# Kernel tuning notes

Hardware: AMD Instinct MI355X
Metric: run time of the kernel (lower is better)

Reference implementation:

```python
import jax, jax.numpy as jnp
import numpy as np

N_NODES = 50000
N_EDGES = 800000
D_IN = 128
D_HID = 128
N_CLASSES = 10


def setup_inputs() -> dict:
    key = jax.random.key(0)
    ks = jax.random.split(key, 8)
    x = jax.random.normal(ks[0], (N_NODES, D_IN), dtype=jnp.float32)
    edge_index = jax.random.randint(ks[1], (2, N_EDGES), 0, N_NODES, dtype=jnp.int64)
    s = 1.0 / np.sqrt(D_IN)
    W1 = jax.random.uniform(ks[2], (D_IN, D_HID), jnp.float32, -s, s)
    b1 = jnp.zeros((D_HID,), jnp.float32)
    W2 = jax.random.uniform(ks[3], (D_HID, D_HID), jnp.float32, -s, s)
    b2 = jnp.zeros((D_HID,), jnp.float32)
    sl = 1.0 / np.sqrt(D_HID)
    Wl = jax.random.uniform(ks[4], (D_HID, N_CLASSES), jnp.float32, -sl, sl)
    bl = jax.random.uniform(ks[5], (N_CLASSES,), jnp.float32, -sl, sl)
    return {"x": x, "edge_index": edge_index, "W1": W1, "b1": b1,
            "W2": W2, "b2": b2, "Wl": Wl, "bl": bl}


def gcn_conv(x, src, dst, W, b, n_nodes):
    # PyG GCNConv: add self-loops, symmetric normalization, gather-scatter aggregate
    h = x @ W                                             # [N, D_out]
    loop = jnp.arange(n_nodes, dtype=src.dtype)
    src2 = jnp.concatenate([src, loop])                   # [E+N]
    dst2 = jnp.concatenate([dst, loop])
    deg = jax.ops.segment_sum(jnp.ones_like(dst2, dtype=h.dtype), dst2,
                              num_segments=n_nodes)       # in-degree incl. self-loop
    dinv = jnp.where(deg > 0, jax.lax.rsqrt(deg), 0.0)
    norm = dinv[src2] * dinv[dst2]                        # [E+N]
    msgs = h[src2] * norm[:, None]                        # gather + scale  [E+N, D_out]
    out = jax.ops.segment_sum(msgs, dst2, num_segments=n_nodes)  # scatter-add
    return out + b


def reference(x, edge_index, W1, b1, W2, b2, Wl, bl):
    src, dst = edge_index[0], edge_index[1]
    n = x.shape[0]
    h = jax.nn.relu(gcn_conv(x, src, dst, W1, b1, n))     # dropout is identity in eval
    h = jax.nn.relu(gcn_conv(h, src, dst, W2, b2, n))
    logits = h @ Wl + bl                                  # [N, C]
    return jax.nn.log_softmax(logits, axis=1)
```

## Files before the change

### kernel.cpp

```cpp
#include <hip/hip_runtime.h>
#include <hip/hip_bf16.h>

#define D 128
#define NCLS 10

static __device__ __forceinline__ float relu(float x){ return fmaxf(x, 0.0f); }
static __device__ __forceinline__ float bf_lo(unsigned v){ return __uint_as_float(v << 16); }
static __device__ __forceinline__ float bf_hi(unsigned v){ return __uint_as_float(v & 0xffff0000u); }

__global__ __launch_bounds__(256) void k_zero_i32(int* __restrict__ p, int n){
  int i = blockIdx.x*256 + threadIdx.x;
  if (i < n) p[i] = 0;
}

__global__ __launch_bounds__(256) void k_hist(const int* __restrict__ dst,
                                              int* __restrict__ counts, int E){
  int i = blockIdx.x*256 + threadIdx.x;
  if (i < E) atomicAdd(counts + dst[i], 1);
}

__global__ __launch_bounds__(256) void k_scan1(const int* __restrict__ counts,
                                               int* __restrict__ rowPtr,
                                               int* __restrict__ bsum, int n){
  const int i = blockIdx.x*256 + threadIdx.x;
  const int lane = threadIdx.x & 63;
  const int wid  = threadIdx.x >> 6;
  int v = (i < n) ? counts[i] : 0;
  int s = v;
  #pragma unroll
  for (int off = 1; off < 64; off <<= 1){
    int u = __shfl_up(s, off, 64);
    if (lane >= off) s += u;
  }
  __shared__ int ws[4];
  if (lane == 63) ws[wid] = s;
  __syncthreads();
  int add = 0;
  if (wid >= 1) add += ws[0];
  if (wid >= 2) add += ws[1];
  if (wid >= 3) add += ws[2];
  int incl = s + add;
  if (i < n) rowPtr[i] = incl - v;
  if (threadIdx.x == 255) bsum[blockIdx.x] = incl;
}

__global__ __launch_bounds__(256) void k_scan2(int* __restrict__ bsum,
                                               int* __restrict__ rowPtr,
                                               int nb, int n){
  const int t = threadIdx.x;
  const int lane = t & 63;
  const int wid  = t >> 6;
  int v = (t < nb) ? bsum[t] : 0;
  int s = v;
  #pragma unroll
  for (int off = 1; off < 64; off <<= 1){
    int u = __shfl_up(s, off, 64);
    if (lane >= off) s += u;
  }
  __shared__ int ws[4];
  if (lane == 63) ws[wid] = s;
  __syncthreads();
  int add = 0;
  if (wid >= 1) add += ws[0];
  if (wid >= 2) add += ws[1];
  if (wid >= 3) add += ws[2];
  int incl = s + add;
  if (t < nb) bsum[t] = incl - v;
  if (t == 255) rowPtr[n] = incl;
}

__global__ __launch_bounds__(256) void k_scan3(const int* __restrict__ counts,
                                               const int* __restrict__ bsum,
                                               int* __restrict__ rowPtr,
                                               float* __restrict__ dinv, int n){
  int i = blockIdx.x*256 + threadIdx.x;
  if (i >= n) return;
  rowPtr[i] += bsum[blockIdx.x];
  dinv[i] = rsqrtf((float)(counts[i] + 1));
}

__global__ __launch_bounds__(256) void k_scatter(const int* __restrict__ src,
                                                 const int* __restrict__ dst,
                                                 const int* __restrict__ rowPtr,
                                                 int* __restrict__ cursor,
                                                 int* __restrict__ srcs, int E){
  int i = blockIdx.x*256 + threadIdx.x;
  if (i >= E) return;
  int d = dst[i];
  int pos = rowPtr[d] + atomicAdd(cursor + d, 1);
  srcs[pos] = src[i];
}

__global__ __launch_bounds__(256) void k_gemm128(const float* __restrict__ A,
                                                 const float* __restrict__ W,
                                                 __hip_bfloat16* __restrict__ C,
                                                 int M, int doRelu){
  __shared__ float4 sW4[64*32];
  __shared__ float4 sA4[32*33];
  const int tid = threadIdx.x;
  const int row0 = blockIdx.x * 32;
  const float4* A4 = (const float4*)A + (size_t)row0 * 32;
  const int rowsHere = (M - row0 >= 32) ? 32 : (M - row0);
  const int nf4 = rowsHere * 32;
  for (int i = tid; i < 32*32; i += 256){
    float4 v = make_float4(0.f, 0.f, 0.f, 0.f);
    if (i < nf4) v = A4[i];
    if (doRelu){ v.x=relu(v.x); v.y=relu(v.y); v.z=relu(v.z); v.w=relu(v.w); }
    sA4[(i >> 5)*33 + (i & 31)] = v;
  }
  const int colg = tid & 15;
  const int rowg = tid >> 4;
  float4 acc00 = make_float4(0,0,0,0), acc01 = acc00, acc10 = acc00, acc11 = acc00;
  for (int ph = 0; ph < 2; ++ph){
    __syncthreads();
    const float4* Wp = (const float4*)W + ph * (64*32);
    #pragma unroll
    for (int i = 0; i < 8; ++i) sW4[i*256 + tid] = Wp[i*256 + tid];
    __syncthreads();
    #pragma unroll 4
    for (int k4 = 0; k4 < 16; ++k4){
      float4 a0 = sA4[(2*rowg)*33   + ph*16 + k4];
      float4 a1 = sA4[(2*rowg+1)*33 + ph*16 + k4];
      #pragma unroll
      for (int kk = 0; kk < 4; ++kk){
        const int k = k4*4 + kk;
        float4 w0 = sW4[k*32 + colg];
        float4 w1 = sW4[k*32 + colg + 16];
        float av0 = ((const float*)&a0)[kk];
        float av1 = ((const float*)&a1)[kk];
        acc00.x += av0*w0.x; acc00.y += av0*w0.y; acc00.z += av0*w0.z; acc00.w += av0*w0.w;
        acc01.x += av0*w1.x; acc01.y += av0*w1.y; acc01.z += av0*w1.z; acc01.w += av0*w1.w;
        acc10.x += av1*w0.x; acc10.y += av1*w0.y; acc10.z += av1*w0.z; acc10.w += av1*w0.w;
        acc11.x += av1*w1.x; acc11.y += av1*w1.y; acc11.z += av1*w1.z; acc11.w += av1*w1.w;
      }
    }
  }
  union Pack { ushort4 u; __hip_bfloat16 b[4]; };
  ushort4* C4 = (ushort4*)C;
  const int r0 = row0 + 2*rowg;
  if (r0 < M){
    Pack p0, p1;
    p0.b[0]=__float2bfloat16(acc00.x); p0.b[1]=__float2bfloat16(acc00.y);
    p0.b[2]=__float2bfloat16(acc00.z); p0.b[3]=__float2bfloat16(acc00.w);
    p1.b[0]=__float2bfloat16(acc01.x); p1.b[1]=__float2bfloat16(acc01.y);
    p1.b[2]=__float2bfloat16(acc01.z); p1.b[3]=__float2bfloat16(acc01.w);
    C4[(size_t)r0*32 + colg]      = p0.u;
    C4[(size_t)r0*32 + colg + 16] = p1.u;
  }
  if (r0 + 1 < M){
    Pack p0, p1;
    p0.b[0]=__float2bfloat16(acc10.x); p0.b[1]=__float2bfloat16(acc10.y);
    p0.b[2]=__float2bfloat16(acc10.z); p0.b[3]=__float2bfloat16(acc10.w);
    p1.b[0]=__float2bfloat16(acc11.x); p1.b[1]=__float2bfloat16(acc11.y);
    p1.b[2]=__float2bfloat16(acc11.z); p1.b[3]=__float2bfloat16(acc11.w);
    C4[(size_t)(r0+1)*32 + colg]      = p0.u;
    C4[(size_t)(r0+1)*32 + colg + 16] = p1.u;
  }
}

#define AGG_CORE_BF16                                                          \
  const int grp = lane >> 4;                                                   \
  const int q   = lane & 15;                                                   \
  float dn = dinv[node];                                                       \
  float4 aA0 = make_float4(0,0,0,0), aB0 = aA0, aA1 = aA0, aB1 = aA0;          \
  int beg = rowPtr[node], end = rowPtr[node+1];                                \
  for (int j = beg; j < end; j += 64){                                         \
    int rem = end - j;                                                         \
    int cnt = (rem < 64) ? rem : 64;                                           \
    int s = 0; float ds = 0.f;                                                 \
    if (lane < cnt){ s = srcs[j + lane]; ds = dinv[s]; }                       \
    int T = (((cnt + 3) >> 2) + 1) & ~1;                                       \
    for (int t = 0; t < T; t += 2){                                            \
      _Pragma("unroll")                                                        \
      for (int u = 0; u < 2; ++u){                                             \
        int e = 4*(t+u) + grp;                                                 \
        int sb = __shfl(s, e);                                                 \
        float nb = __shfl(ds, e) * dn;                                         \
        uint4 hv = ((const uint4*)(h + (size_t)sb*D))[q];                      \
        float4& cA = u ? aA1 : aA0;                                            \
        float4& cB = u ? aB1 : aB0;                                            \
        cA.x += bf_lo(hv.x)*nb; cA.y += bf_hi(hv.x)*nb;                        \
        cA.z += bf_lo(hv.y)*nb; cA.w += bf_hi(hv.y)*nb;                        \
        cB.x += bf_lo(hv.z)*nb; cB.y += bf_hi(hv.z)*nb;                        \
        cB.z += bf_lo(hv.w)*nb; cB.w += bf_hi(hv.w)*nb;                        \
      }                                                                        \
    }                                                                          \
  }                                                                            \
  float4 rA, rB;                                                               \
  rA.x=aA0.x+aA1.x; rA.y=aA0.y+aA1.y; rA.z=aA0.z+aA1.z; rA.w=aA0.w+aA1.w;      \
  rB.x=aB0.x+aB1.x; rB.y=aB0.y+aB1.y; rB.z=aB0.z+aB1.z; rB.w=aB0.w+aB1.w;      \
  rA.x += __shfl_xor(rA.x,16,64); rA.y += __shfl_xor(rA.y,16,64);              \
  rA.z += __shfl_xor(rA.z,16,64); rA.w += __shfl_xor(rA.w,16,64);              \
  rB.x += __shfl_xor(rB.x,16,64); rB.y += __shfl_xor(rB.y,16,64);              \
  rB.z += __shfl_xor(rB.z,16,64); rB.w += __shfl_xor(rB.w,16,64);              \
  rA.x += __shfl_xor(rA.x,32,64); rA.y += __shfl_xor(rA.y,32,64);              \
  rA.z += __shfl_xor(rA.z,32,64); rA.w += __shfl_xor(rA.w,32,64);              \
  rB.x += __shfl_xor(rB.x,32,64); rB.y += __shfl_xor(rB.y,32,64);              \
  rB.z += __shfl_xor(rB.z,32,64); rB.w += __shfl_xor(rB.w,32,64);

__global__ __launch_bounds__(256) void k_agg_csr(const ushort* __restrict__ h,
                                                 const int* __restrict__ rowPtr,
                                                 const int* __restrict__ srcs,
                                                 const float* __restrict__ dinv,
                                                 const float* __restrict__ b,
                                                 float* __restrict__ out, int n){
  int gid = blockIdx.x*256 + threadIdx.x;
  int node = gid >> 6;
  int lane = gid & 63;
  if (node >= n) return;
  AGG_CORE_BF16
  if (grp != 0) return;
  uint4 hs = ((const uint4*)(h + (size_t)node*D))[q];
  float sl = dn * dn;
  float4 bA = ((const float4*)b)[2*q];
  float4 bB = ((const float4*)b)[2*q + 1];
  rA.x += bf_lo(hs.x)*sl + bA.x; rA.y += bf_hi(hs.x)*sl + bA.y;
  rA.z += bf_lo(hs.y)*sl + bA.z; rA.w += bf_hi(hs.y)*sl + bA.w;
  rB.x += bf_lo(hs.z)*sl + bB.x; rB.y += bf_hi(hs.z)*sl + bB.y;
  rB.z += bf_lo(hs.w)*sl + bB.w - bB.w + bB.z; rB.w += bf_hi(hs.w)*sl + bB.w;
  float4* o4 = (float4*)(out + (size_t)node*D);
  o4[2*q]     = rA;
  o4[2*q + 1] = rB;
}

__global__ __launch_bounds__(256) void k_agg_head(const ushort* __restrict__ h,
                                                  const int* __restrict__ rowPtr,
                                                  const int* __restrict__ srcs,
                                                  const float* __restrict__ dinv,
                                                  const float* __restrict__ b,
                                                  const float* __restrict__ Wl,
                                                  const float* __restrict__ bl,
                                                  float* __restrict__ out, int n){
  int gid = blockIdx.x*256 + threadIdx.x;
  int node = gid >> 6;
  int lane = gid & 63;
  if (node >= n) return;
  AGG_CORE_BF16
  if (grp != 0) return;
  uint4 hs = ((const uint4*)(h + (size_t)node*D))[q];
  float sl = dn * dn;
  float4 bA = ((const float4*)b)[2*q];
  float4 bB = ((const float4*)b)[2*q + 1];
  float r[8];
  r[0] = relu(rA.x + bf_lo(hs.x)*sl + bA.x);
  r[1] = relu(rA.y + bf_hi(hs.x)*sl + bA.y);
  r[2] = relu(rA.z + bf_lo(hs.y)*sl + bA.z);
  r[3] = relu(rA.w + bf_hi(hs.y)*sl + bA.w);
  r[4] = relu(rB.x + bf_lo(hs.z)*sl + bB.x);
  r[5] = relu(rB.y + bf_hi(hs.z)*sl + bB.y);
  r[6] = relu(rB.z + bf_lo(hs.w)*sl + bB.z);
  r[7] = relu(rB.w + bf_hi(hs.w)*sl + bB.w);
  float lacc[NCLS];
  #pragma unroll
  for (int c = 0; c < NCLS; ++c){
    float a = 0.f;
    #pragma unroll
    for (int i = 0; i < 8; ++i) a += r[i] * Wl[(8*q + i)*NCLS + c];
    lacc[c] = a;
  }
  #pragma unroll
  for (int c = 0; c < NCLS; ++c){
    #pragma unroll
    for (int off = 8; off >= 1; off >>= 1)
      lacc[c] += __shfl_xor(lacc[c], off, 16);
    lacc[c] += bl[c];
  }
  float m = lacc[0];
  #pragma unroll
  for (int c = 1; c < NCLS; ++c) m = fmaxf(m, lacc[c]);
  float se = 0.f;
  #pragma unroll
  for (int c = 0; c < NCLS; ++c) se += expf(lacc[c] - m);
  float lse = m + logf(se);
  if (q < NCLS){
    float v = lacc[0];
    #pragma unroll
    for (int c = 1; c < NCLS; ++c) if (q == c) v = lacc[c];
    out[(size_t)node*NCLS + q] = v - lse;
  }
}

extern "C" void kernel_launch(void* const* d_in, const int* in_sizes, int n_in,
                              void* d_out, int out_size, void* d_ws, size_t ws_size,
                              hipStream_t stream){
  const float* x  = (const float*)d_in[0];
  const int*   ei = (const int*)d_in[1];
  const float* W1 = (const float*)d_in[2];
  const float* b1 = (const float*)d_in[3];
  const float* W2 = (const float*)d_in[4];
  const float* b2 = (const float*)d_in[5];
  const float* Wl = (const float*)d_in[6];
  const float* bl = (const float*)d_in[7];
  float* out = (float*)d_out;

  const int N = in_sizes[0] / D;
  const int E = in_sizes[1] / 2;
  const int* src = ei;
  const int* dst = ei + E;

  char* ws = (char*)d_ws;
  size_t off = 0;
  ushort* hbuf  = (ushort*)(ws + off); off += (size_t)N*D*2;
  float* bufB   = (float*)(ws + off);  off += (size_t)N*D*4;
  int*   counts = (int*)(ws + off);    off += (size_t)N*4;
  int*   cursor = (int*)(ws + off);    off += (size_t)N*4;
  int*   rowPtr = (int*)(ws + off);    off += (size_t)(N+1)*4;
  float* dinv   = (float*)(ws + off);  off += (size_t)N*4;
  int*   bsum   = (int*)(ws + off);    off += (size_t)256*4;
  int*   srcs   = (int*)(ws + off);    off += (size_t)E*4;

  const int nbN   = (N + 255)/256;
  const int nb2N  = (2*N + 255)/256;
  const int nbE   = (E + 255)/256;
  const int gemmB = (N + 31)/32;
  const int aggB  = (N + 3)/4;

  k_zero_i32<<<nb2N, 256, 0, stream>>>(counts, 2*N);
  k_hist<<<nbE, 256, 0, stream>>>(dst, counts, E);
  k_scan1<<<nbN, 256, 0, stream>>>(counts, rowPtr, bsum, N);
  k_scan2<<<1, 256, 0, stream>>>(bsum, rowPtr, nbN, N);
  k_scan3<<<nbN, 256, 0, stream>>>(counts, bsum, rowPtr, dinv, N);
  k_scatter<<<nbE, 256, 0, stream>>>(src, dst, rowPtr, cursor, srcs, E);

  k_gemm128<<<gemmB, 256, 0, stream>>>(x, W1, (__hip_bfloat16*)hbuf, N, 0);
  k_agg_csr<<<aggB, 256, 0, stream>>>(hbuf, rowPtr, srcs, dinv, b1, bufB, N);

  k_gemm128<<<gemmB, 256, 0, stream>>>(bufB, W2, (__hip_bfloat16*)hbuf, N, 1);
  k_agg_head<<<aggB, 256, 0, stream>>>(hbuf, rowPtr, srcs, dinv, b2, Wl, bl, out, N);
}
```

Baseline: 255.1 us.

## Pack edge src with dinv, store layer-1 output as bf16, deepen aggregation ILP

The scatter step now writes each edge's source index together with that source's dinv as an int2, so the aggregation no longer does a dependent random dinv gather per edge. The layer-1 aggregation writes bf16 instead of fp32, which halves that intermediate's write and its re-read by a new bf16-input GEMM variant. The aggregation loop now keeps four independent accumulator pairs instead of two, giving more loads in flight. dinv is computed inside scan1 rather than scan3. The trade-offs are more registers in the aggregation, a second lossy bf16 rounding of the hidden activations, and double-size edge records.

```diff
diff --git a/kernel.cpp b/kernel.cpp
--- a/kernel.cpp
+++ b/kernel.cpp
@@ -21,11 +21,13 @@
 
 __global__ __launch_bounds__(256) void k_scan1(const int* __restrict__ counts,
                                                int* __restrict__ rowPtr,
-                                               int* __restrict__ bsum, int n){
+                                               int* __restrict__ bsum,
+                                               float* __restrict__ dinv, int n){
   const int i = blockIdx.x*256 + threadIdx.x;
   const int lane = threadIdx.x & 63;
   const int wid  = threadIdx.x >> 6;
   int v = (i < n) ? counts[i] : 0;
+  if (i < n) dinv[i] = rsqrtf((float)(v + 1));
   int s = v;
   #pragma unroll
   for (int off = 1; off < 64; off <<= 1){
@@ -69,29 +71,28 @@
   if (t == 255) rowPtr[n] = incl;
 }
 
-__global__ __launch_bounds__(256) void k_scan3(const int* __restrict__ counts,
-                                               const int* __restrict__ bsum,
-                                               int* __restrict__ rowPtr,
-                                               float* __restrict__ dinv, int n){
+__global__ __launch_bounds__(256) void k_scan3(const int* __restrict__ bsum,
+                                               int* __restrict__ rowPtr, int n){
   int i = blockIdx.x*256 + threadIdx.x;
-  if (i >= n) return;
-  rowPtr[i] += bsum[blockIdx.x];
-  dinv[i] = rsqrtf((float)(counts[i] + 1));
+  if (i < n) rowPtr[i] += bsum[blockIdx.x];
 }
 
 __global__ __launch_bounds__(256) void k_scatter(const int* __restrict__ src,
                                                  const int* __restrict__ dst,
                                                  const int* __restrict__ rowPtr,
+                                                 const float* __restrict__ dinv,
                                                  int* __restrict__ cursor,
-                                                 int* __restrict__ srcs, int E){
+                                                 int2* __restrict__ edat, int E){
   int i = blockIdx.x*256 + threadIdx.x;
   if (i >= E) return;
   int d = dst[i];
+  int s = src[i];
   int pos = rowPtr[d] + atomicAdd(cursor + d, 1);
-  srcs[pos] = src[i];
-}
-
-__global__ __launch_bounds__(256) void k_gemm128(const float* __restrict__ A,
+  edat[pos] = make_int2(s, __float_as_int(dinv[s]));
+}
+
+template<bool BF16IN>
+__global__ __launch_bounds__(256) void k_gemm128(const void* __restrict__ Av,
                                                  const float* __restrict__ W,
                                                  __hip_bfloat16* __restrict__ C,
                                                  int M, int doRelu){
@@ -99,14 +100,33 @@
   __shared__ float4 sA4[32*33];
   const int tid = threadIdx.x;
   const int row0 = blockIdx.x * 32;
-  const float4* A4 = (const float4*)A + (size_t)row0 * 32;
   const int rowsHere = (M - row0 >= 32) ? 32 : (M - row0);
-  const int nf4 = rowsHere * 32;
-  for (int i = tid; i < 32*32; i += 256){
-    float4 v = make_float4(0.f, 0.f, 0.f, 0.f);
-    if (i < nf4) v = A4[i];
-    if (doRelu){ v.x=relu(v.x); v.y=relu(v.y); v.z=relu(v.z); v.w=relu(v.w); }
-    sA4[(i >> 5)*33 + (i & 31)] = v;
+  if (BF16IN){
+    const uint4* A8 = (const uint4*)((const ushort*)Av + (size_t)row0 * D);
+    for (int i = tid; i < 32*16; i += 256){
+      int r = i >> 4, c8 = i & 15;
+      float4 lo = make_float4(0,0,0,0), hi = lo;
+      if (r < rowsHere){
+        uint4 v = A8[i];
+        lo.x = bf_lo(v.x); lo.y = bf_hi(v.x); lo.z = bf_lo(v.y); lo.w = bf_hi(v.y);
+        hi.x = bf_lo(v.z); hi.y = bf_hi(v.z); hi.z = bf_lo(v.w); hi.w = bf_hi(v.w);
+        if (doRelu){
+          lo.x=relu(lo.x); lo.y=relu(lo.y); lo.z=relu(lo.z); lo.w=relu(lo.w);
+          hi.x=relu(hi.x); hi.y=relu(hi.y); hi.z=relu(hi.z); hi.w=relu(hi.w);
+        }
+      }
+      sA4[r*33 + 2*c8]     = lo;
+      sA4[r*33 + 2*c8 + 1] = hi;
+    }
+  } else {
+    const float4* A4 = (const float4*)Av + (size_t)row0 * 32;
+    const int nf4 = rowsHere * 32;
+    for (int i = tid; i < 32*32; i += 256){
+      float4 v = make_float4(0.f, 0.f, 0.f, 0.f);
+      if (i < nf4) v = A4[i];
+      if (doRelu){ v.x=relu(v.x); v.y=relu(v.y); v.z=relu(v.z); v.w=relu(v.w); }
+      sA4[(i >> 5)*33 + (i & 31)] = v;
+    }
   }
   const int colg = tid & 15;
   const int rowg = tid >> 4;
@@ -162,23 +182,24 @@
   const int grp = lane >> 4;                                                   \
   const int q   = lane & 15;                                                   \
   float dn = dinv[node];                                                       \
-  float4 aA0 = make_float4(0,0,0,0), aB0 = aA0, aA1 = aA0, aB1 = aA0;          \
+  float4 aA0 = make_float4(0,0,0,0), aB0 = aA0;                                \
+  float4 aA1 = aA0, aB1 = aA0, aA2 = aA0, aB2 = aA0, aA3 = aA0, aB3 = aA0;     \
   int beg = rowPtr[node], end = rowPtr[node+1];                                \
   for (int j = beg; j < end; j += 64){                                         \
     int rem = end - j;                                                         \
     int cnt = (rem < 64) ? rem : 64;                                           \
-    int s = 0; float ds = 0.f;                                                 \
-    if (lane < cnt){ s = srcs[j + lane]; ds = dinv[s]; }                       \
-    int T = (((cnt + 3) >> 2) + 1) & ~1;                                       \
-    for (int t = 0; t < T; t += 2){                                            \
+    int2 ed = make_int2(0, 0);                                                 \
+    if (lane < cnt) ed = edat[j + lane];                                       \
+    int T = (((cnt + 3) >> 2) + 3) & ~3;                                       \
+    for (int t = 0; t < T; t += 4){                                            \
       _Pragma("unroll")                                                        \
-      for (int u = 0; u < 2; ++u){                                             \
+      for (int u = 0; u < 4; ++u){                                             \
         int e = 4*(t+u) + grp;                                                 \
-        int sb = __shfl(s, e);                                                 \
-        float nb = __shfl(ds, e) * dn;                                         \
+        int sb = __shfl(ed.x, e);                                              \
+        float nb = __uint_as_float((unsigned)__shfl(ed.y, e)) * dn;            \
         uint4 hv = ((const uint4*)(h + (size_t)sb*D))[q];                      \
-        float4& cA = u ? aA1 : aA0;                                            \
-        float4& cB = u ? aB1 : aB0;                                            \
+        float4& cA = (u==0)?aA0:(u==1)?aA1:(u==2)?aA2:aA3;                     \
+        float4& cB = (u==0)?aB0:(u==1)?aB1:(u==2)?aB2:aB3;                     \
         cA.x += bf_lo(hv.x)*nb; cA.y += bf_hi(hv.x)*nb;                        \
         cA.z += bf_lo(hv.y)*nb; cA.w += bf_hi(hv.y)*nb;                        \
         cB.x += bf_lo(hv.z)*nb; cB.y += bf_hi(hv.z)*nb;                        \
@@ -187,8 +208,10 @@
     }                                                                          \
   }                                                                            \
   float4 rA, rB;                                                               \
-  rA.x=aA0.x+aA1.x; rA.y=aA0.y+aA1.y; rA.z=aA0.z+aA1.z; rA.w=aA0.w+aA1.w;      \
-  rB.x=aB0.x+aB1.x; rB.y=aB0.y+aB1.y; rB.z=aB0.z+aB1.z; rB.w=aB0.w+aB1.w;      \
+  rA.x=(aA0.x+aA1.x)+(aA2.x+aA3.x); rA.y=(aA0.y+aA1.y)+(aA2.y+aA3.y);          \
+  rA.z=(aA0.z+aA1.z)+(aA2.z+aA3.z); rA.w=(aA0.w+aA1.w)+(aA2.w+aA3.w);          \
+  rB.x=(aB0.x+aB1.x)+(aB2.x+aB3.x); rB.y=(aB0.y+aB1.y)+(aB2.y+aB3.y);          \
+  rB.z=(aB0.z+aB1.z)+(aB2.z+aB3.z); rB.w=(aB0.w+aB1.w)+(aB2.w+aB3.w);          \
   rA.x += __shfl_xor(rA.x,16,64); rA.y += __shfl_xor(rA.y,16,64);              \
   rA.z += __shfl_xor(rA.z,16,64); rA.w += __shfl_xor(rA.w,16,64);              \
   rB.x += __shfl_xor(rB.x,16,64); rB.y += __shfl_xor(rB.y,16,64);              \
@@ -200,10 +223,10 @@
 
 __global__ __launch_bounds__(256) void k_agg_csr(const ushort* __restrict__ h,
                                                  const int* __restrict__ rowPtr,
-                                                 const int* __restrict__ srcs,
+                                                 const int2* __restrict__ edat,
                                                  const float* __restrict__ dinv,
                                                  const float* __restrict__ b,
-                                                 float* __restrict__ out, int n){
+                                                 ushort* __restrict__ out, int n){
   int gid = blockIdx.x*256 + threadIdx.x;
   int node = gid >> 6;
   int lane = gid & 63;
@@ -214,18 +237,24 @@
   float sl = dn * dn;
   float4 bA = ((const float4*)b)[2*q];
   float4 bB = ((const float4*)b)[2*q + 1];
-  rA.x += bf_lo(hs.x)*sl + bA.x; rA.y += bf_hi(hs.x)*sl + bA.y;
-  rA.z += bf_lo(hs.y)*sl + bA.z; rA.w += bf_hi(hs.y)*sl + bA.w;
-  rB.x += bf_lo(hs.z)*sl + bB.x; rB.y += bf_hi(hs.z)*sl + bB.y;
-  rB.z += bf_lo(hs.w)*sl + bB.w - bB.w + bB.z; rB.w += bf_hi(hs.w)*sl + bB.w;
-  float4* o4 = (float4*)(out + (size_t)node*D);
-  o4[2*q]     = rA;
-  o4[2*q + 1] = rB;
+  float r[8];
+  r[0] = rA.x + bf_lo(hs.x)*sl + bA.x;
+  r[1] = rA.y + bf_hi(hs.x)*sl + bA.y;
+  r[2] = rA.z + bf_lo(hs.y)*sl + bA.z;
+  r[3] = rA.w + bf_hi(hs.y)*sl + bA.w;
+  r[4] = rB.x + bf_lo(hs.z)*sl + bB.x;
+  r[5] = rB.y + bf_hi(hs.z)*sl + bB.y;
+  r[6] = rB.z + bf_lo(hs.w)*sl + bB.z;
+  r[7] = rB.w + bf_hi(hs.w)*sl + bB.w;
+  union Pack { uint4 u; __hip_bfloat16 b[8]; } p;
+  #pragma unroll
+  for (int i = 0; i < 8; ++i) p.b[i] = __float2bfloat16(r[i]);
+  ((uint4*)(out + (size_t)node*D))[q] = p.u;
 }
 
 __global__ __launch_bounds__(256) void k_agg_head(const ushort* __restrict__ h,
                                                   const int* __restrict__ rowPtr,
-                                                  const int* __restrict__ srcs,
+                                                  const int2* __restrict__ edat,
                                                   const float* __restrict__ dinv,
                                                   const float* __restrict__ b,
                                                   const float* __restrict__ Wl,
@@ -300,14 +329,15 @@
 
   char* ws = (char*)d_ws;
   size_t off = 0;
-  ushort* hbuf  = (ushort*)(ws + off); off += (size_t)N*D*2;
-  float* bufB   = (float*)(ws + off);  off += (size_t)N*D*4;
+  ushort* h1    = (ushort*)(ws + off); off += (size_t)N*D*2;
+  ushort* g1    = (ushort*)(ws + off); off += (size_t)N*D*2;
+  ushort* h2    = (ushort*)(ws + off); off += (size_t)N*D*2;
   int*   counts = (int*)(ws + off);    off += (size_t)N*4;
   int*   cursor = (int*)(ws + off);    off += (size_t)N*4;
   int*   rowPtr = (int*)(ws + off);    off += (size_t)(N+1)*4;
   float* dinv   = (float*)(ws + off);  off += (size_t)N*4;
   int*   bsum   = (int*)(ws + off);    off += (size_t)256*4;
-  int*   srcs   = (int*)(ws + off);    off += (size_t)E*4;
+  int2*  edat   = (int2*)(ws + off);   off += (size_t)E*8;
 
   const int nbN   = (N + 255)/256;
   const int nb2N  = (2*N + 255)/256;
@@ -317,14 +347,14 @@
 
   k_zero_i32<<<nb2N, 256, 0, stream>>>(counts, 2*N);
   k_hist<<<nbE, 256, 0, stream>>>(dst, counts, E);
-  k_scan1<<<nbN, 256, 0, stream>>>(counts, rowPtr, bsum, N);
+  k_scan1<<<nbN, 256, 0, stream>>>(counts, rowPtr, bsum, dinv, N);
   k_scan2<<<1, 256, 0, stream>>>(bsum, rowPtr, nbN, N);
-  k_scan3<<<nbN, 256, 0, stream>>>(counts, bsum, rowPtr, dinv, N);
-  k_scatter<<<nbE, 256, 0, stream>>>(src, dst, rowPtr, cursor, srcs, E);
-
-  k_gemm128<<<gemmB, 256, 0, stream>>>(x, W1, (__hip_bfloat16*)hbuf, N, 0);
-  k_agg_csr<<<aggB, 256, 0, stream>>>(hbuf, rowPtr, srcs, dinv, b1, bufB, N);
-
-  k_gemm128<<<gemmB, 256, 0, stream>>>(bufB, W2, (__hip_bfloat16*)hbuf, N, 1);
-  k_agg_head<<<aggB, 256, 0, stream>>>(hbuf, rowPtr, srcs, dinv, b2, Wl, bl, out, N);
-}
+  k_scan3<<<nbN, 256, 0, stream>>>(bsum, rowPtr, N);
+  k_scatter<<<nbE, 256, 0, stream>>>(src, dst, rowPtr, dinv, cursor, edat, E);
+
+  k_gemm128<false><<<gemmB, 256, 0, stream>>>(x, W1, (__hip_bfloat16*)h1, N, 0);
+  k_agg_csr<<<aggB, 256, 0, stream>>>(h1, rowPtr, edat, dinv, b1, g1, N);
+
+  k_gemm128<true><<<gemmB, 256, 0, stream>>>(g1, W2, (__hip_bfloat16*)h2, N, 1);
+  k_agg_head<<<aggB, 256, 0, stream>>>(h2, rowPtr, edat, dinv, b2, Wl, bl, out, N);
+}
```

New measurement: 262.5 us. +2.9%, slower.
